# Optimization experiments

Measured on AMD Instinct MI355X. Metric: run time of the kernel, lower is better.

Reference implementation:

```python
import jax, jax.numpy as jnp
import numpy as np

N_PATCHES = 14
PS = 32                      # patch size = 448 // 14
HIDDEN = 64
N_HEADS = 4
DH = HIDDEN // N_HEADS       # 16
N_BLOCKS = 2
INPUT_D = PS * PS            # c=1 -> 1024
MLP_R = 4
EPS = 1e-5                   # nn.LayerNorm default


def _pos_emb(S, d):
    # get_positional_embeddings: sin(i/10000**(j/d)) for even j, cos(i/10000**((j-1)/d)) for odd j
    i = jnp.arange(S, dtype=jnp.float32)[:, None]
    j = jnp.arange(d, dtype=jnp.float32)[None, :]
    even = (jnp.arange(d) % 2 == 0)[None, :]
    ae = i / jnp.power(jnp.float32(10000.0), j / d)
    ao = i / jnp.power(jnp.float32(10000.0), (j - 1.0) / d)
    return jnp.where(even, jnp.sin(ae), jnp.cos(ao))


def _patchify(images):
    # [n,c,h,w] -> [n, n_patches^2, c*ps*ps]; patch flattened in (c, row, col) order as in torch .flatten()
    n, c, h, w = images.shape
    x = images.reshape(n, c, N_PATCHES, PS, N_PATCHES, PS)
    x = x.transpose(0, 2, 4, 1, 3, 5)            # [n, pi, pj, c, ps, ps]
    return x.reshape(n, N_PATCHES * N_PATCHES, c * PS * PS)


def _depatchify(p):
    # inverse of _patchify with c=1 (as the original depatchify derives c = np2/n_patches^2 = 1)
    n = p.shape[0]
    x = p.reshape(n, N_PATCHES, N_PATCHES, 1, PS, PS)
    x = x.transpose(0, 3, 1, 4, 2, 5)
    return x.reshape(n, 1, N_PATCHES * PS, N_PATCHES * PS)


def _ln(x, g, b):
    m = x.mean(-1, keepdims=True)
    v = ((x - m) ** 2).mean(-1, keepdims=True)
    return (x - m) / jnp.sqrt(v + EPS) * g + b


def _msa(x, Wq, bq, Wk, bk, Wv, bv):
    # batched over sequences and heads; equivalent to the original per-seq/per-head python loops
    n, S, d = x.shape
    xh = x.reshape(n, S, N_HEADS, DH)
    q = jnp.einsum('nshd,hde->nshe', xh, Wq) + bq
    k = jnp.einsum('nshd,hde->nshe', xh, Wk) + bk
    v = jnp.einsum('nshd,hde->nshe', xh, Wv) + bv
    att = jax.nn.softmax(jnp.einsum('nshe,nthe->nhst', q, k) / jnp.sqrt(jnp.float32(DH)), axis=-1)
    o = jnp.einsum('nhst,nthe->nshe', att, v)    # [n,S,h,dh]
    return o.reshape(n, S, d)                    # hstack over heads == contiguous head layout


def _block(x, p, i):
    h = x + _msa(_ln(x, p['ln1_g'][i], p['ln1_b'][i]),
                 p['Wq'][i], p['bq'][i], p['Wk'][i], p['bk'][i], p['Wv'][i], p['bv'][i])
    z = _ln(h, p['ln2_g'][i], p['ln2_b'][i])
    z = jax.nn.gelu(z @ p['W1'][i] + p['b1'][i], approximate=False) @ p['W2'][i] + p['b2'][i]
    return h + z


def setup_inputs() -> dict:
    key = jax.random.key(0)
    ks = iter(jax.random.split(key, 80))
    def rn(shape, s=0.02):
        return jax.random.normal(next(ks), shape, dtype=jnp.float32) * s
    N = 128
    inp = {
        'images': jax.random.normal(next(ks), (N, 1, 448, 448), dtype=jnp.float32),
        'class_token': jax.random.uniform(next(ks), (1, HIDDEN), dtype=jnp.float32),  # torch.rand init
        'lm_W': rn((INPUT_D, HIDDEN)), 'lm_b': jnp.zeros((HIDDEN,), jnp.float32),
        'lm2_W': rn((HIDDEN, INPUT_D)), 'lm2_b': jnp.zeros((INPUT_D,), jnp.float32),
        'mlp1_W': rn((HIDDEN, 1)), 'mlp1_b': jnp.zeros((1,), jnp.float32),
        'mlp4_W': rn((1, HIDDEN)), 'mlp4_b': jnp.zeros((HIDDEN,), jnp.float32),
    }
    for pre in ('enc_', 'dec_'):
        inp[pre + 'ln1_g'] = jnp.ones((N_BLOCKS, HIDDEN), jnp.float32)
        inp[pre + 'ln1_b'] = jnp.zeros((N_BLOCKS, HIDDEN), jnp.float32)
        inp[pre + 'ln2_g'] = jnp.ones((N_BLOCKS, HIDDEN), jnp.float32)
        inp[pre + 'ln2_b'] = jnp.zeros((N_BLOCKS, HIDDEN), jnp.float32)
        for nm in ('Wq', 'Wk', 'Wv'):
            inp[pre + nm] = rn((N_BLOCKS, N_HEADS, DH, DH), 0.05)
        for nm in ('bq', 'bk', 'bv'):
            inp[pre + nm] = jnp.zeros((N_BLOCKS, N_HEADS, DH), jnp.float32)
        inp[pre + 'W1'] = rn((N_BLOCKS, HIDDEN, MLP_R * HIDDEN))
        inp[pre + 'b1'] = jnp.zeros((N_BLOCKS, MLP_R * HIDDEN), jnp.float32)
        inp[pre + 'W2'] = rn((N_BLOCKS, MLP_R * HIDDEN, HIDDEN))
        inp[pre + 'b2'] = jnp.zeros((N_BLOCKS, HIDDEN), jnp.float32)
    return inp


def reference(images, class_token, lm_W, lm_b, lm2_W, lm2_b,
              mlp1_W, mlp1_b, mlp4_W, mlp4_b,
              enc_ln1_g, enc_ln1_b, enc_ln2_g, enc_ln2_b,
              enc_Wq, enc_bq, enc_Wk, enc_bk, enc_Wv, enc_bv,
              enc_W1, enc_b1, enc_W2, enc_b2,
              dec_ln1_g, dec_ln1_b, dec_ln2_g, dec_ln2_b,
              dec_Wq, dec_bq, dec_Wk, dec_bk, dec_Wv, dec_bv,
              dec_W1, dec_b1, dec_W2, dec_b2):
    n = images.shape[0]
    patches = _patchify(images)                            # [n, 196, 1024]
    tokens = patches @ lm_W + lm_b                         # [n, 196, 64]
    cls = jnp.broadcast_to(class_token[None], (n, 1, HIDDEN))
    out = jnp.concatenate([cls, tokens], axis=1)           # [n, 197, 64]
    out = out + _pos_emb(N_PATCHES ** 2 + 1, HIDDEN)[None]
    enc = dict(ln1_g=enc_ln1_g, ln1_b=enc_ln1_b, ln2_g=enc_ln2_g, ln2_b=enc_ln2_b,
               Wq=enc_Wq, bq=enc_bq, Wk=enc_Wk, bk=enc_bk, Wv=enc_Wv, bv=enc_bv,
               W1=enc_W1, b1=enc_b1, W2=enc_W2, b2=enc_b2)
    for i in range(N_BLOCKS):
        out = _block(out, enc, i)
    lat = jax.nn.gelu(out[:, 1:, :] @ mlp1_W + mlp1_b, approximate=False)   # [n, 196, 1]
    out = jax.nn.gelu(lat @ mlp4_W + mlp4_b, approximate=False)             # [n, 196, 64]
    dec = dict(ln1_g=dec_ln1_g, ln1_b=dec_ln1_b, ln2_g=dec_ln2_g, ln2_b=dec_ln2_b,
               Wq=dec_Wq, bq=dec_bq, Wk=dec_Wk, bk=dec_bk, Wv=dec_Wv, bv=dec_bv,
               W1=dec_W1, b1=dec_b1, W2=dec_W2, b2=dec_b2)
    for i in range(N_BLOCKS):
        out = _block(out, dec, i)
    out = out + _pos_emb(N_PATCHES ** 2, HIDDEN)[None]
    out = out @ lm2_W + lm2_b                              # [n, 196, 1024]
    reimage = _depatchify(out)                             # [n, 1, 448, 448]
    return (lat, reimage)
```

## Files before the change

kernel.cpp:

```cpp
#include <hip/hip_runtime.h>
#include <math.h>

#define N_IMG 128
#define EPS 1e-5f

__device__ __forceinline__ float gelu_f(float x) {
    return 0.5f * x * (1.0f + erff(x * 0.70710678118654752f));
}

__device__ __forceinline__ float wave_sum(float v) {
    #pragma unroll
    for (int m = 1; m < 64; m <<= 1) v += __shfl_xor(v, m);
    return v;
}

__device__ __forceinline__ void fma4(float4& acc, float s, const float4& v) {
    acc.x += s * v.x; acc.y += s * v.y; acc.z += s * v.z; acc.w += s * v.w;
}

__device__ __forceinline__ float dot4(const float4& a, const float4& b) {
    return a.x * b.x + a.y * b.y + a.z * b.z + a.w * b.w;
}

__global__ void k_posemb(float* __restrict__ pe) {
    int idx = blockIdx.x * 256 + threadIdx.x;
    if (idx >= 197 * 64) return;
    int i = idx >> 6, j = idx & 63;
    int jj = j & ~1;
    float inv = powf(10000.0f, (float)jj / 64.0f);
    float a = (float)i / inv;
    pe[idx] = (j & 1) ? cosf(a) : sinf(a);
}

__global__ __launch_bounds__(256, 2) void k_patch(
    const float* __restrict__ img, const float* __restrict__ W,
    const float* __restrict__ bias, const float* __restrict__ pe,
    float* __restrict__ x)
{
    __shared__ float As[64 * 44];
    __shared__ float Bs[32 * 76];
    int tid = threadIdx.x;
    int tx = tid & 15, ty = tid >> 4;
    int m0 = blockIdx.x * 64;

    int ra = tid >> 2, ca = (tid & 3) * 8;
    int rowa = m0 + ra;
    int na = rowa / 196, pa = rowa - na * 196;
    const float* abase = img + (size_t)na * 200704 + (pa / 14) * (32 * 448) + (pa % 14) * 32 + ca;

    int kr = tid >> 3, cb = (tid & 7) * 8;

    float4 acc[4];
    #pragma unroll
    for (int i = 0; i < 4; ++i) acc[i] = make_float4(0.f, 0.f, 0.f, 0.f);

    for (int kc = 0; kc < 32; ++kc) {
        float4 a0 = *(const float4*)(abase + kc * 448);
        float4 a1 = *(const float4*)(abase + kc * 448 + 4);
        const float* wp = W + (size_t)(kc * 32 + kr) * 64 + cb;
        float4 b0 = *(const float4*)(wp);
        float4 b1 = *(const float4*)(wp + 4);
        __syncthreads();
        *(float4*)&As[ra * 44 + ca]     = a0;
        *(float4*)&As[ra * 44 + ca + 4] = a1;
        *(float4*)&Bs[kr * 76 + cb]     = b0;
        *(float4*)&Bs[kr * 76 + cb + 4] = b1;
        __syncthreads();
        #pragma unroll 4
        for (int k4 = 0; k4 < 8; ++k4) {
            float4 a[4], b[4];
            #pragma unroll
            for (int i = 0; i < 4; ++i) a[i] = *(float4*)&As[(ty + 16 * i) * 44 + k4 * 4];
            #pragma unroll
            for (int kk = 0; kk < 4; ++kk) b[kk] = *(float4*)&Bs[(k4 * 4 + kk) * 76 + tx * 4];
            #pragma unroll
            for (int i = 0; i < 4; ++i) {
                fma4(acc[i], a[i].x, b[0]);
                fma4(acc[i], a[i].y, b[1]);
                fma4(acc[i], a[i].z, b[2]);
                fma4(acc[i], a[i].w, b[3]);
            }
        }
    }
    int col = tx * 4;
    float4 bb = *(const float4*)(bias + col);
    #pragma unroll
    for (int i = 0; i < 4; ++i) {
        int row = m0 + ty + 16 * i;
        int n = row / 196, p = row - n * 196;
        float4 pv = *(const float4*)(pe + (size_t)(1 + p) * 64 + col);
        float4 o;
        o.x = acc[i].x + bb.x + pv.x;
        o.y = acc[i].y + bb.y + pv.y;
        o.z = acc[i].z + bb.z + pv.z;
        o.w = acc[i].w + bb.w + pv.w;
        *(float4*)&x[((size_t)(n * 197 + 1 + p)) * 64 + col] = o;
    }
}

__global__ void k_cls(const float* __restrict__ cls, const float* __restrict__ pe,
                      float* __restrict__ x) {
    int idx = blockIdx.x * 256 + threadIdx.x;
    if (idx >= 128 * 64) return;
    int n = idx >> 6, j = idx & 63;
    x[(size_t)n * 197 * 64 + j] = cls[j] + pe[j];
}

__global__ __launch_bounds__(256, 2) void k_ln_qkv(
    const float* __restrict__ x, const float* __restrict__ g, const float* __restrict__ bta,
    const float* __restrict__ Wq, const float* __restrict__ bq,
    const float* __restrict__ Wk, const float* __restrict__ bk,
    const float* __restrict__ Wv, const float* __restrict__ bv,
    float* __restrict__ q, float* __restrict__ k, float* __restrict__ v, int S)
{
    __shared__ float z[4][64];
    int tid = threadIdx.x, w = tid >> 6, l = tid & 63;
    int row = blockIdx.x * 4 + w;
    if (row >= N_IMG * S) return;
    float xv = x[(size_t)row * 64 + l];
    float m = wave_sum(xv) * (1.0f / 64.0f);
    float t = xv - m;
    float var = wave_sum(t * t) * (1.0f / 64.0f);
    float zv = t * rsqrtf(var + EPS) * g[l] + bta[l];
    z[w][l] = zv;
    int h = l >> 4, e = l & 15;
    const float* zh = &z[w][h * 16];
    const float* wq = Wq + h * 256 + e;
    const float* wk = Wk + h * 256 + e;
    const float* wv = Wv + h * 256 + e;
    float aq = bq[l], ak = bk[l], av = bv[l];
    #pragma unroll
    for (int d = 0; d < 16; ++d) {
        float zd = zh[d];
        aq += zd * wq[d * 16];
        ak += zd * wk[d * 16];
        av += zd * wv[d * 16];
    }
    int n = row / S, s = row - n * S;
    size_t o = ((size_t)((n * 4 + h) * S + s)) * 16 + e;
    q[o] = aq; k[o] = ak; v[o] = av;
}

struct KV { float4 k[2][4]; float4 v[2][4]; };

__device__ __forceinline__ void ld_pair(KV& b, const float* kp, const float* vp, int j) {
    #pragma unroll
    for (int u = 0; u < 2; ++u) {
        #pragma unroll
        for (int c = 0; c < 4; ++c) {
            b.k[u][c] = *(const float4*)(kp + (size_t)(j + u) * 16 + c * 4);
            b.v[u][c] = *(const float4*)(vp + (size_t)(j + u) * 16 + c * 4);
        }
    }
}

__device__ __forceinline__ void comp_one(const KV& b, int u, const float4* qv,
                                         float& l, float4* o) {
    float sc = dot4(qv[0], b.k[u][0]) + dot4(qv[1], b.k[u][1]) +
               dot4(qv[2], b.k[u][2]) + dot4(qv[3], b.k[u][3]);
    float p = __expf(sc);
    l += p;
    fma4(o[0], p, b.v[u][0]); fma4(o[1], p, b.v[u][1]);
    fma4(o[2], p, b.v[u][2]); fma4(o[3], p, b.v[u][3]);
}

__global__ __launch_bounds__(256, 2) void k_attn(
    const float* __restrict__ q, const float* __restrict__ k, const float* __restrict__ v,
    const float* __restrict__ x, float* __restrict__ hout, int S)
{
    int h = blockIdx.x & 3, n = blockIdx.x >> 2;
    int tid = threadIdx.x;
    int s = tid < S ? tid : S - 1;
    const float* qrow = q + ((size_t)((n * 4 + h) * S + s)) * 16;
    float4 qv[4];
    #pragma unroll
    for (int c = 0; c < 4; ++c) {
        float4 t = *(const float4*)(qrow + c * 4);
        t.x *= 0.25f; t.y *= 0.25f; t.z *= 0.25f; t.w *= 0.25f;
        qv[c] = t;
    }
    const float* kp = k + (size_t)(n * 4 + h) * S * 16;
    const float* vp = v + (size_t)(n * 4 + h) * S * 16;
    float l = 0.0f;
    float4 o[4];
    #pragma unroll
    for (int c = 0; c < 4; ++c) o[c] = make_float4(0.f, 0.f, 0.f, 0.f);

    KV A, B;
    ld_pair(A, kp, vp, 0);
    int j = 0;
    for (; j + 4 <= S; j += 4) {
        ld_pair(B, kp, vp, j + 2);
        comp_one(A, 0, qv, l, o);
        comp_one(A, 1, qv, l, o);
        ld_pair(A, kp, vp, j + 4);
        comp_one(B, 0, qv, l, o);
        comp_one(B, 1, qv, l, o);
    }
    int rem = S - j;
    if (rem > 0) comp_one(A, 0, qv, l, o);
    if (rem > 1) comp_one(A, 1, qv, l, o);
    if (rem > 2) {
        ld_pair(B, kp, vp, j + 2);
        comp_one(B, 0, qv, l, o);
    }

    float rl = 1.0f / l;
    if (tid < S) {
        size_t base = ((size_t)n * S + tid) * 64 + h * 16;
        #pragma unroll
        for (int e4 = 0; e4 < 4; ++e4) {
            float4 xv = *(const float4*)(x + base + e4 * 4);
            float4 w;
            w.x = xv.x + o[e4].x * rl;
            w.y = xv.y + o[e4].y * rl;
            w.z = xv.z + o[e4].z * rl;
            w.w = xv.w + o[e4].w * rl;
            *(float4*)(hout + base + e4 * 4) = w;
        }
    }
}

__global__ __launch_bounds__(256, 4) void k_mlp1(
    const float* __restrict__ hbuf, const float* __restrict__ g, const float* __restrict__ bta,
    const float* __restrict__ W1, const float* __restrict__ b1,
    float* __restrict__ mid)
{
    __shared__ float As[64 * 76];
    __shared__ float Bs[64 * 76];
    int tid = threadIdx.x;
    int tx = tid & 15, ty = tid >> 4;
    int m0 = blockIdx.x * 64;
    int nc = blockIdx.y;
    int r = tid >> 2, cpart = (tid & 3) * 16;
    {
        const float* hp = hbuf + ((size_t)(m0 + r)) * 64 + cpart;
        float4 hv[4];
        #pragma unroll
        for (int i = 0; i < 4; ++i) hv[i] = *(const float4*)(hp + i * 4);
        float ps = 0.f;
        #pragma unroll
        for (int i = 0; i < 4; ++i) ps += hv[i].x + hv[i].y + hv[i].z + hv[i].w;
        ps += __shfl_xor(ps, 1); ps += __shfl_xor(ps, 2);
        float mean = ps * (1.0f / 64.0f);
        float vs = 0.f;
        #pragma unroll
        for (int i = 0; i < 4; ++i) {
            float dx = hv[i].x - mean, dy = hv[i].y - mean, dz = hv[i].z - mean, dw = hv[i].w - mean;
            vs += dx * dx + dy * dy + dz * dz + dw * dw;
        }
        vs += __shfl_xor(vs, 1); vs += __shfl_xor(vs, 2);
        float rstd = rsqrtf(vs * (1.0f / 64.0f) + EPS);
        #pragma unroll
        for (int i = 0; i < 4; ++i) {
            float4 gv = *(const float4*)(g + cpart + i * 4);
            float4 bv = *(const float4*)(bta + cpart + i * 4);
            float4 zv;
            zv.x = (hv[i].x - mean) * rstd * gv.x + bv.x;
            zv.y = (hv[i].y - mean) * rstd * gv.y + bv.y;
            zv.z = (hv[i].z - mean) * rstd * gv.z + bv.z;
            zv.w = (hv[i].w - mean) * rstd * gv.w + bv.w;
            *(float4*)&As[r * 76 + cpart + i * 4] = zv;
        }
    }
    const float* wp = W1 + (size_t)r * 256 + nc * 64 + cpart;
    float4 wv4[4];
    #pragma unroll
    for (int i = 0; i < 4; ++i) wv4[i] = *(const float4*)(wp + i * 4);
    __syncthreads();
    #pragma unroll
    for (int i = 0; i < 4; ++i)
        *(float4*)&Bs[r * 76 + cpart + i * 4] = wv4[i];
    __syncthreads();
    float4 acc[4];
    #pragma unroll
    for (int i = 0; i < 4; ++i) acc[i] = make_float4(0.f, 0.f, 0.f, 0.f);
    #pragma unroll 4
    for (int k4 = 0; k4 < 16; ++k4) {
        float4 a[4], b[4];
        #pragma unroll
        for (int i = 0; i < 4; ++i) a[i] = *(float4*)&As[(ty + 16 * i) * 76 + k4 * 4];
        #pragma unroll
        for (int kk = 0; kk < 4; ++kk) b[kk] = *(float4*)&Bs[(k4 * 4 + kk) * 76 + tx * 4];
        #pragma unroll
        for (int i = 0; i < 4; ++i) {
            fma4(acc[i], a[i].x, b[0]);
            fma4(acc[i], a[i].y, b[1]);
            fma4(acc[i], a[i].z, b[2]);
            fma4(acc[i], a[i].w, b[3]);
        }
    }
    int col = nc * 64 + tx * 4;
    float4 b1v = *(const float4*)(b1 + col);
    #pragma unroll
    for (int i = 0; i < 4; ++i) {
        int row = m0 + ty + 16 * i;
        float4 ov;
        ov.x = gelu_f(acc[i].x + b1v.x);
        ov.y = gelu_f(acc[i].y + b1v.y);
        ov.z = gelu_f(acc[i].z + b1v.z);
        ov.w = gelu_f(acc[i].w + b1v.w);
        *(float4*)&mid[(size_t)row * 256 + col] = ov;
    }
}

__global__ __launch_bounds__(256, 4) void k_mlp2(
    const float* __restrict__ mid, const float* __restrict__ W2, const float* __restrict__ b2,
    const float* __restrict__ hbuf, float* __restrict__ out)
{
    __shared__ float As[64 * 76];
    __shared__ float Bs[64 * 76];
    int tid = threadIdx.x;
    int tx = tid & 15, ty = tid >> 4;
    int m0 = blockIdx.x * 64;
    int r = tid >> 2, cpart = (tid & 3) * 16;
    float4 acc[4];
    #pragma unroll
    for (int i = 0; i < 4; ++i) acc[i] = make_float4(0.f, 0.f, 0.f, 0.f);
    for (int kc = 0; kc < 4; ++kc) {
        const float* mp = mid + ((size_t)(m0 + r)) * 256 + kc * 64 + cpart;
        float4 av[4];
        #pragma unroll
        for (int i = 0; i < 4; ++i) av[i] = *(const float4*)(mp + i * 4);
        const float* wp = W2 + (size_t)(kc * 64 + r) * 64 + cpart;
        float4 wv4[4];
        #pragma unroll
        for (int i = 0; i < 4; ++i) wv4[i] = *(const float4*)(wp + i * 4);
        __syncthreads();
        #pragma unroll
        for (int i = 0; i < 4; ++i) {
            *(float4*)&As[r * 76 + cpart + i * 4] = av[i];
            *(float4*)&Bs[r * 76 + cpart + i * 4] = wv4[i];
        }
        __syncthreads();
        #pragma unroll 4
        for (int k4 = 0; k4 < 16; ++k4) {
            float4 a[4], b[4];
            #pragma unroll
            for (int i = 0; i < 4; ++i) a[i] = *(float4*)&As[(ty + 16 * i) * 76 + k4 * 4];
            #pragma unroll
            for (int kk = 0; kk < 4; ++kk) b[kk] = *(float4*)&Bs[(k4 * 4 + kk) * 76 + tx * 4];
            #pragma unroll
            for (int i = 0; i < 4; ++i) {
                fma4(acc[i], a[i].x, b[0]);
                fma4(acc[i], a[i].y, b[1]);
                fma4(acc[i], a[i].z, b[2]);
                fma4(acc[i], a[i].w, b[3]);
            }
        }
    }
    int col = tx * 4;
    float4 b2v = *(const float4*)(b2 + col);
    #pragma unroll
    for (int i = 0; i < 4; ++i) {
        int row = m0 + ty + 16 * i;
        float4 hv = *(const float4*)(hbuf + (size_t)row * 64 + col);
        float4 ov;
        ov.x = acc[i].x + b2v.x + hv.x;
        ov.y = acc[i].y + b2v.y + hv.y;
        ov.z = acc[i].z + b2v.z + hv.z;
        ov.w = acc[i].w + b2v.w + hv.w;
        *(float4*)&out[(size_t)row * 64 + col] = ov;
    }
}

__global__ __launch_bounds__(256) void k_bneck(
    const float* __restrict__ xenc, const float* __restrict__ m1W, const float* __restrict__ m1b,
    const float* __restrict__ m4W, const float* __restrict__ m4b,
    float* __restrict__ lat_out, float* __restrict__ xdec)
{
    int tid = threadIdx.x, w = tid >> 6, l = tid & 63;
    int row = blockIdx.x * 4 + w;
    if (row >= 128 * 196) return;
    int n = row / 196, p = row - n * 196;
    float xv = xenc[((size_t)(n * 197 + 1 + p)) * 64 + l];
    float sum = wave_sum(xv * m1W[l]);
    float lat = gelu_f(sum + m1b[0]);
    if (l == 0) lat_out[row] = lat;
    float ov = gelu_f(lat * m4W[l] + m4b[l]);
    xdec[(size_t)row * 64 + l] = ov;
}

__global__ __launch_bounds__(256, 4) void k_final(
    const float* __restrict__ xdec, const float* __restrict__ pe,
    const float* __restrict__ W, const float* __restrict__ bias,
    float* __restrict__ img_out)
{
    __shared__ float As[64 * 76];
    __shared__ float Bs[64 * 76];
    int tid = threadIdx.x;
    int tx = tid & 15, ty = tid >> 4;
    int m0 = blockIdx.x * 64;
    int r = tid >> 2, cpart = (tid & 3) * 16;
    {
        int row = m0 + r;
        int n = row / 196, p = row - n * 196;
        const float* xp = xdec + (size_t)row * 64 + cpart;
        const float* pp = pe + (size_t)p * 64 + cpart;
        #pragma unroll
        for (int i = 0; i < 4; ++i) {
            float4 xv = *(const float4*)(xp + i * 4);
            float4 pv = *(const float4*)(pp + i * 4);
            float4 zv;
            zv.x = xv.x + pv.x; zv.y = xv.y + pv.y; zv.z = xv.z + pv.z; zv.w = xv.w + pv.w;
            *(float4*)&As[r * 76 + cpart + i * 4] = zv;
        }
    }
    for (int t = 0; t < 4; ++t) {
        int nb = blockIdx.y * 4 + t;
        const float* wp = W + (size_t)r * 1024 + nb * 64 + cpart;
        float4 wv4[4];
        #pragma unroll
        for (int i = 0; i < 4; ++i) wv4[i] = *(const float4*)(wp + i * 4);
        __syncthreads();
        #pragma unroll
        for (int i = 0; i < 4; ++i)
            *(float4*)&Bs[r * 76 + cpart + i * 4] = wv4[i];
        __syncthreads();
        float4 acc[4];
        #pragma unroll
        for (int i = 0; i < 4; ++i) acc[i] = make_float4(0.f, 0.f, 0.f, 0.f);
        #pragma unroll 4
        for (int k4 = 0; k4 < 16; ++k4) {
            float4 a[4], b[4];
            #pragma unroll
            for (int i = 0; i < 4; ++i) a[i] = *(float4*)&As[(ty + 16 * i) * 76 + k4 * 4];
            #pragma unroll
            for (int kk = 0; kk < 4; ++kk) b[kk] = *(float4*)&Bs[(k4 * 4 + kk) * 76 + tx * 4];
            #pragma unroll
            for (int i = 0; i < 4; ++i) {
                fma4(acc[i], a[i].x, b[0]);
                fma4(acc[i], a[i].y, b[1]);
                fma4(acc[i], a[i].z, b[2]);
                fma4(acc[i], a[i].w, b[3]);
            }
        }
        int colj = nb * 64 + tx * 4;
        float4 bv = *(const float4*)(bias + colj);
        int rr = colj >> 5, cc = colj & 31;
        #pragma unroll
        for (int i = 0; i < 4; ++i) {
            int row = m0 + ty + 16 * i;
            int n = row / 196, p = row - n * 196;
            int pi = p / 14, pj = p - pi * 14;
            size_t off = (size_t)n * 200704 + (size_t)(pi * 32 + rr) * 448 + pj * 32 + cc;
            float4 ov;
            ov.x = acc[i].x + bv.x;
            ov.y = acc[i].y + bv.y;
            ov.z = acc[i].z + bv.z;
            ov.w = acc[i].w + bv.w;
            *(float4*)&img_out[off] = ov;
        }
    }
}

extern "C" void kernel_launch(void* const* d_in, const int* in_sizes, int n_in,
                              void* d_out, int out_size, void* d_ws, size_t ws_size,
                              hipStream_t stream) {
    const float* images = (const float*)d_in[0];
    const float* cls    = (const float*)d_in[1];
    const float* lm_W   = (const float*)d_in[2];
    const float* lm_b   = (const float*)d_in[3];
    const float* lm2_W  = (const float*)d_in[4];
    const float* lm2_b  = (const float*)d_in[5];
    const float* m1W    = (const float*)d_in[6];
    const float* m1b    = (const float*)d_in[7];
    const float* m4W    = (const float*)d_in[8];
    const float* m4b    = (const float*)d_in[9];

    float* pe   = (float*)d_ws;
    float* xb   = pe + 12608;
    float* hb   = xb + 1614848;
    float* qb   = hb + 1614848;
    float* kb   = qb + 1614848;
    float* vb   = kb + 1614848;
    float* midb = vb + 1614848;

    float* lat_out = (float*)d_out;
    float* img_out = (float*)d_out + 25088;

    hipLaunchKernelGGL(k_posemb, dim3(50), dim3(256), 0, stream, pe);
    hipLaunchKernelGGL(k_patch, dim3(392), dim3(256), 0, stream, images, lm_W, lm_b, pe, xb);
    hipLaunchKernelGGL(k_cls, dim3(32), dim3(256), 0, stream, cls, pe, xb);

    float* cur_x = xb;
    float* cur_h = hb;
    for (int grp = 0; grp < 2; ++grp) {
        int base = 10 + grp * 14;
        const float* ln1_g = (const float*)d_in[base + 0];
        const float* ln1_b = (const float*)d_in[base + 1];
        const float* ln2_g = (const float*)d_in[base + 2];
        const float* ln2_b = (const float*)d_in[base + 3];
        const float* Wq = (const float*)d_in[base + 4];
        const float* Wk = (const float*)d_in[base + 5];
        const float* Wv = (const float*)d_in[base + 6];
        const float* bq = (const float*)d_in[base + 7];
        const float* bk = (const float*)d_in[base + 8];
        const float* bv = (const float*)d_in[base + 9];
        const float* W1 = (const float*)d_in[base + 10];
        const float* b1 = (const float*)d_in[base + 11];
        const float* W2 = (const float*)d_in[base + 12];
        const float* b2 = (const float*)d_in[base + 13];
        int S = (grp == 0) ? 197 : 196;
        int rows = 128 * S;
        for (int i = 0; i < 2; ++i) {
            hipLaunchKernelGGL(k_ln_qkv, dim3(rows / 4), dim3(256), 0, stream,
                cur_x, ln1_g + i * 64, ln1_b + i * 64,
                Wq + i * 1024, bq + i * 64, Wk + i * 1024, bk + i * 64,
                Wv + i * 1024, bv + i * 64, qb, kb, vb, S);
            hipLaunchKernelGGL(k_attn, dim3(512), dim3(256), 0, stream,
                qb, kb, vb, cur_x, cur_h, S);
            hipLaunchKernelGGL(k_mlp1, dim3(rows / 64, 4), dim3(256), 0, stream,
                cur_h, ln2_g + i * 64, ln2_b + i * 64, W1 + i * 16384, b1 + i * 256, midb);
            hipLaunchKernelGGL(k_mlp2, dim3(rows / 64), dim3(256), 0, stream,
                midb, W2 + i * 16384, b2 + i * 64, cur_h, cur_x);
        }
        if (grp == 0) {
            hipLaunchKernelGGL(k_bneck, dim3(6272), dim3(256), 0, stream,
                cur_x, m1W, m1b, m4W, m4b, lat_out, hb);
            cur_x = hb;
            cur_h = xb;
        }
    }
    hipLaunchKernelGGL(k_final, dim3(392, 4), dim3(256), 0, stream, cur_x, pe, lm2_W, lm2_b, img_out);
}
```

Baseline: 884.2 us.

## Split patch-embed GEMM over K with combine kernel; halve mlp2 row tile

After: 874.6 us. Within noise of the previous version (-1.1%).

```diff
diff --git a/kernel.cpp b/kernel.cpp
--- a/kernel.cpp
+++ b/kernel.cpp
@@ -3,6 +3,7 @@
 
 #define N_IMG 128
 #define EPS 1e-5f
+#define PART_STRIDE 1614848
 
 __device__ __forceinline__ float gelu_f(float x) {
     return 0.5f * x * (1.0f + erff(x * 0.70710678118654752f));
@@ -32,16 +33,16 @@
     pe[idx] = (j & 1) ? cosf(a) : sinf(a);
 }
 
-__global__ __launch_bounds__(256, 2) void k_patch(
+__global__ __launch_bounds__(256, 6) void k_patch(
     const float* __restrict__ img, const float* __restrict__ W,
-    const float* __restrict__ bias, const float* __restrict__ pe,
-    float* __restrict__ x)
+    float* __restrict__ part)
 {
     __shared__ float As[64 * 44];
     __shared__ float Bs[32 * 76];
     int tid = threadIdx.x;
     int tx = tid & 15, ty = tid >> 4;
     int m0 = blockIdx.x * 64;
+    int kc0 = blockIdx.y * 8;
 
     int ra = tid >> 2, ca = (tid & 3) * 8;
     int rowa = m0 + ra;
@@ -54,7 +55,8 @@
     #pragma unroll
     for (int i = 0; i < 4; ++i) acc[i] = make_float4(0.f, 0.f, 0.f, 0.f);
 
-    for (int kc = 0; kc < 32; ++kc) {
+    for (int it = 0; it < 8; ++it) {
+        int kc = kc0 + it;
         float4 a0 = *(const float4*)(abase + kc * 448);
         float4 a1 = *(const float4*)(abase + kc * 448 + 4);
         const float* wp = W + (size_t)(kc * 32 + kr) * 64 + cb;
@@ -82,20 +84,35 @@
             }
         }
     }
+    float* pp = part + (size_t)blockIdx.y * PART_STRIDE;
     int col = tx * 4;
-    float4 bb = *(const float4*)(bias + col);
     #pragma unroll
     for (int i = 0; i < 4; ++i) {
         int row = m0 + ty + 16 * i;
-        int n = row / 196, p = row - n * 196;
-        float4 pv = *(const float4*)(pe + (size_t)(1 + p) * 64 + col);
-        float4 o;
-        o.x = acc[i].x + bb.x + pv.x;
-        o.y = acc[i].y + bb.y + pv.y;
-        o.z = acc[i].z + bb.z + pv.z;
-        o.w = acc[i].w + bb.w + pv.w;
-        *(float4*)&x[((size_t)(n * 197 + 1 + p)) * 64 + col] = o;
-    }
+        *(float4*)&pp[(size_t)row * 64 + col] = acc[i];
+    }
+}
+
+__global__ __launch_bounds__(256) void k_pcomb(
+    const float* __restrict__ part, const float* __restrict__ bias,
+    const float* __restrict__ pe, float* __restrict__ x)
+{
+    int idx = blockIdx.x * 256 + threadIdx.x;
+    int row = idx >> 4, c4 = (idx & 15) * 4;
+    int n = row / 196, p = row - n * 196;
+    const float* p0 = part + (size_t)row * 64 + c4;
+    float4 a = *(const float4*)(p0);
+    float4 b = *(const float4*)(p0 + PART_STRIDE);
+    float4 c = *(const float4*)(p0 + 2 * (size_t)PART_STRIDE);
+    float4 d = *(const float4*)(p0 + 3 * (size_t)PART_STRIDE);
+    float4 bb = *(const float4*)(bias + c4);
+    float4 pv = *(const float4*)(pe + (size_t)(1 + p) * 64 + c4);
+    float4 o;
+    o.x = a.x + b.x + c.x + d.x + bb.x + pv.x;
+    o.y = a.y + b.y + c.y + d.y + bb.y + pv.y;
+    o.z = a.z + b.z + c.z + d.z + bb.z + pv.z;
+    o.w = a.w + b.w + c.w + d.w + bb.w + pv.w;
+    *(float4*)&x[((size_t)(n * 197 + 1 + p)) * 64 + c4] = o;
 }
 
 __global__ void k_cls(const float* __restrict__ cls, const float* __restrict__ pe,
@@ -308,40 +325,40 @@
     const float* __restrict__ mid, const float* __restrict__ W2, const float* __restrict__ b2,
     const float* __restrict__ hbuf, float* __restrict__ out)
 {
-    __shared__ float As[64 * 76];
+    __shared__ float As[32 * 76];
     __shared__ float Bs[64 * 76];
     int tid = threadIdx.x;
     int tx = tid & 15, ty = tid >> 4;
-    int m0 = blockIdx.x * 64;
-    int r = tid >> 2, cpart = (tid & 3) * 16;
-    float4 acc[4];
-    #pragma unroll
-    for (int i = 0; i < 4; ++i) acc[i] = make_float4(0.f, 0.f, 0.f, 0.f);
+    int m0 = blockIdx.x * 32;
+    int ra = tid >> 3, ca = (tid & 7) * 8;
+    int rb = tid >> 2, cb = (tid & 3) * 16;
+    float4 acc[2];
+    acc[0] = make_float4(0.f, 0.f, 0.f, 0.f);
+    acc[1] = make_float4(0.f, 0.f, 0.f, 0.f);
     for (int kc = 0; kc < 4; ++kc) {
-        const float* mp = mid + ((size_t)(m0 + r)) * 256 + kc * 64 + cpart;
-        float4 av[4];
-        #pragma unroll
-        for (int i = 0; i < 4; ++i) av[i] = *(const float4*)(mp + i * 4);
-        const float* wp = W2 + (size_t)(kc * 64 + r) * 64 + cpart;
+        const float* mp = mid + ((size_t)(m0 + ra)) * 256 + kc * 64 + ca;
+        float4 av0 = *(const float4*)(mp);
+        float4 av1 = *(const float4*)(mp + 4);
+        const float* wp = W2 + (size_t)(kc * 64 + rb) * 64 + cb;
         float4 wv4[4];
         #pragma unroll
         for (int i = 0; i < 4; ++i) wv4[i] = *(const float4*)(wp + i * 4);
         __syncthreads();
-        #pragma unroll
-        for (int i = 0; i < 4; ++i) {
-            *(float4*)&As[r * 76 + cpart + i * 4] = av[i];
-            *(float4*)&Bs[r * 76 + cpart + i * 4] = wv4[i];
-        }
+        *(float4*)&As[ra * 76 + ca]     = av0;
+        *(float4*)&As[ra * 76 + ca + 4] = av1;
+        #pragma unroll
+        for (int i = 0; i < 4; ++i)
+            *(float4*)&Bs[rb * 76 + cb + i * 4] = wv4[i];
         __syncthreads();
         #pragma unroll 4
         for (int k4 = 0; k4 < 16; ++k4) {
-            float4 a[4], b[4];
-            #pragma unroll
-            for (int i = 0; i < 4; ++i) a[i] = *(float4*)&As[(ty + 16 * i) * 76 + k4 * 4];
+            float4 a[2], b[4];
+            a[0] = *(float4*)&As[ty * 76 + k4 * 4];
+            a[1] = *(float4*)&As[(ty + 16) * 76 + k4 * 4];
             #pragma unroll
             for (int kk = 0; kk < 4; ++kk) b[kk] = *(float4*)&Bs[(k4 * 4 + kk) * 76 + tx * 4];
             #pragma unroll
-            for (int i = 0; i < 4; ++i) {
+            for (int i = 0; i < 2; ++i) {
                 fma4(acc[i], a[i].x, b[0]);
                 fma4(acc[i], a[i].y, b[1]);
                 fma4(acc[i], a[i].z, b[2]);
@@ -352,7 +369,7 @@
     int col = tx * 4;
     float4 b2v = *(const float4*)(b2 + col);
     #pragma unroll
-    for (int i = 0; i < 4; ++i) {
+    for (int i = 0; i < 2; ++i) {
         int row = m0 + ty + 16 * i;
         float4 hv = *(const float4*)(hbuf + (size_t)row * 64 + col);
         float4 ov;
@@ -480,7 +497,8 @@
     float* img_out = (float*)d_out + 25088;
 
     hipLaunchKernelGGL(k_posemb, dim3(50), dim3(256), 0, stream, pe);
-    hipLaunchKernelGGL(k_patch, dim3(392), dim3(256), 0, stream, images, lm_W, lm_b, pe, xb);
+    hipLaunchKernelGGL(k_patch, dim3(392, 4), dim3(256), 0, stream, images, lm_W, qb);
+    hipLaunchKernelGGL(k_pcomb, dim3(1568), dim3(256), 0, stream, qb, lm_b, pe, xb);
     hipLaunchKernelGGL(k_cls, dim3(32), dim3(256), 0, stream, cls, pe, xb);
 
     float* cur_x = xb;
@@ -512,7 +530,7 @@
                 qb, kb, vb, cur_x, cur_h, S);
             hipLaunchKernelGGL(k_mlp1, dim3(rows / 64, 4), dim3(256), 0, stream,
                 cur_h, ln2_g + i * 64, ln2_b + i * 64, W1 + i * 16384, b1 + i * 256, midb);
-            hipLaunchKernelGGL(k_mlp2, dim3(rows / 64), dim3(256), 0, stream,
+            hipLaunchKernelGGL(k_mlp2, dim3(rows / 32), dim3(256), 0, stream,
                 midb, W2 + i * 16384, b2 + i * 64, cur_h, cur_x);
         }
         if (grp == 0) {
```
